# Kernel tuning notes

Measured on AMD Instinct MI355X. Metric: run time of the kernel, lower is better.

Reference implementation:

```python
import jax, jax.numpy as jnp
import numpy as np

B, T, I, H, L = 64, 1024, 64, 512, 2


def setup_inputs() -> dict:
    key = jax.random.key(0)
    ks = jax.random.split(key, 4 * L + 4)
    k = 1.0 / np.sqrt(H)
    inp = {"x": jax.random.normal(ks[0], (B, T, I), dtype=jnp.float32)}
    in_sizes = [I] + [H] * (L - 1)
    for l in range(L):
        base = 1 + 4 * l
        inp[f"w_ih{l}"] = jax.random.uniform(ks[base + 0], (3 * H, in_sizes[l]), minval=-k, maxval=k, dtype=jnp.float32)
        inp[f"w_hh{l}"] = jax.random.uniform(ks[base + 1], (3 * H, H), minval=-k, maxval=k, dtype=jnp.float32)
        inp[f"b_ih{l}"] = jax.random.uniform(ks[base + 2], (3 * H,), minval=-k, maxval=k, dtype=jnp.float32)
        inp[f"b_hh{l}"] = jax.random.uniform(ks[base + 3], (3 * H,), minval=-k, maxval=k, dtype=jnp.float32)
    kf = 1.0 / np.sqrt(H)
    inp["fc_w"] = jax.random.uniform(ks[-2], (I, H), minval=-kf, maxval=kf, dtype=jnp.float32)
    inp["fc_b"] = jax.random.uniform(ks[-1], (I,), minval=-kf, maxval=kf, dtype=jnp.float32)
    return inp


def _gru_layer(x, w_ih, w_hh, b_ih, b_hh):
    # x: [B, T, in]; precompute input-side gates as one big GEMM
    xg = jnp.einsum('bti,gi->btg', x, w_ih) + b_ih  # [B, T, 3H]
    h0 = jnp.zeros((x.shape[0], w_hh.shape[1]), x.dtype)

    def step(h, xg_t):
        hg = h @ w_hh.T + b_hh                     # [B, 3H]
        xr, xz, xn = jnp.split(xg_t, 3, axis=-1)
        hr, hz, hn = jnp.split(hg, 3, axis=-1)
        r = jax.nn.sigmoid(xr + hr)
        z = jax.nn.sigmoid(xz + hz)
        n = jnp.tanh(xn + r * hn)
        h_new = (1.0 - z) * n + z * h
        return h_new, h_new

    _, ys = jax.lax.scan(step, h0, jnp.swapaxes(xg, 0, 1))  # ys: [T, B, H]
    return jnp.swapaxes(ys, 0, 1)


def reference(x, w_ih0, w_hh0, b_ih0, b_hh0, w_ih1, w_hh1, b_ih1, b_hh1, fc_w, fc_b):
    h = _gru_layer(x, w_ih0, w_hh0, b_ih0, b_hh0)
    h = _gru_layer(h, w_ih1, w_hh1, b_ih1, b_hh1)
    return h @ fc_w.T + fc_b
```

## Files before the change

kernel.cpp:

```cpp
#include <hip/hip_runtime.h>
#include <hip/hip_bf16.h>

#define T_TOTAL 1024
#define BATCH   64
#define HID     512

__device__ __forceinline__ float fast_sigmoid(float x) {
    return 1.f / (1.f + __expf(-x));
}
__device__ __forceinline__ float fast_tanh(float x) {
    float ax = fabsf(x);
    float e  = __expf(-2.f * ax);
    float t  = (1.f - e) / (1.f + e);
    return copysignf(t, x);
}

template<int BM, int BN, int TM, int TN>
__global__ __launch_bounds__(256, 2)
void gemm_bt_k(const float* __restrict__ A, const float* __restrict__ W,
               const float* __restrict__ bias, float* __restrict__ C,
               int K, int T, int Tc, int t0, int N)
{
    constexpr int BK = 16;
    constexpr int WSTR = BN + (BN / 32) * 4;
    static_assert(BM / TM == 16 && BN / TN == 16, "256 threads required");
    __shared__ float As[BK][BM + 4];
    __shared__ float Ws[BK][WSTR];

    const int tid = threadIdx.x;
    const int tx  = tid & 15;
    const int ty  = tid >> 4;
    const int m0  = blockIdx.y * BM;
    const int n0  = blockIdx.x * BN;
    const int nA  = tx * TN;
    const int nsw = nA + ((nA >> 5) << 2);

    float acc[TM][TN];
#pragma unroll
    for (int i = 0; i < TM; ++i)
#pragma unroll
        for (int j = 0; j < TN; ++j) acc[i][j] = 0.f;

    for (int k0 = 0; k0 < K; k0 += BK) {
#pragma unroll
        for (int i = 0; i < (BM * BK) / 1024; ++i) {
            int id = tid + (i << 8);
            int m  = id >> 2;
            int kq = (id & 3) << 2;
            int mloc = m0 + m;
            int rowg = (mloc / Tc) * T + t0 + (mloc % Tc);
            const float4 v = *reinterpret_cast<const float4*>(A + (size_t)rowg * K + k0 + kq);
            As[kq + 0][m] = v.x; As[kq + 1][m] = v.y;
            As[kq + 2][m] = v.z; As[kq + 3][m] = v.w;
        }
#pragma unroll
        for (int i = 0; i < (BN * BK) / 1024; ++i) {
            int id = tid + (i << 8);
            int n  = id >> 2;
            int kq = (id & 3) << 2;
            const float4 v = *reinterpret_cast<const float4*>(W + (size_t)(n0 + n) * K + k0 + kq);
            int np = n + ((n >> 5) << 2);
            Ws[kq + 0][np] = v.x; Ws[kq + 1][np] = v.y;
            Ws[kq + 2][np] = v.z; Ws[kq + 3][np] = v.w;
        }
        __syncthreads();
#pragma unroll
        for (int k = 0; k < BK; ++k) {
            float a[TM], b[TN];
#pragma unroll
            for (int i = 0; i < TM; i += 4)
                *reinterpret_cast<float4*>(&a[i]) =
                    *reinterpret_cast<const float4*>(&As[k][ty * TM + i]);
#pragma unroll
            for (int j = 0; j < TN; j += 4)
                *reinterpret_cast<float4*>(&b[j]) =
                    *reinterpret_cast<const float4*>(&Ws[k][nsw + j]);
#pragma unroll
            for (int i = 0; i < TM; ++i)
#pragma unroll
                for (int j = 0; j < TN; ++j)
                    acc[i][j] = fmaf(a[i], b[j], acc[i][j]);
        }
        __syncthreads();
    }
#pragma unroll
    for (int i = 0; i < TM; ++i) {
        const size_t crow = (size_t)(m0 + ty * TM + i) * N + n0 + nA;
#pragma unroll
        for (int j = 0; j < TN; j += 4) {
            float4 bv = *reinterpret_cast<const float4*>(bias + n0 + nA + j);
            float4 v;
            v.x = acc[i][j + 0] + bv.x; v.y = acc[i][j + 1] + bv.y;
            v.z = acc[i][j + 2] + bv.z; v.w = acc[i][j + 3] + bv.w;
            *reinterpret_cast<float4*>(C + crow + j) = v;
        }
    }
}

__global__ __launch_bounds__(512, 2)
void gru_scan(const float* __restrict__ xg,
              const float* __restrict__ w_hh,
              const float* __restrict__ b_hh,
              float* __restrict__ y,
              unsigned long long* __restrict__ hbuf,
              int t0, int Tc, int tagbase)
{
    const int tid = threadIdx.x;
    const int grp = blockIdx.x & 31;
    const int os  = blockIdx.x >> 5;
    const int D0  = os << 6;
    const int d   = tid & 63;
    const int kc  = tid >> 6;
    const int bg  = grp << 1;

    __shared__ float h_lds[2][1024];
    __shared__ float part[2][8 * 392];

    float4 w4[3][16];
#pragma unroll
    for (int g = 0; g < 3; ++g) {
        const float* wr = w_hh + (size_t)(g * 512 + D0 + d) * 512 + kc * 64;
#pragma unroll
        for (int j = 0; j < 16; ++j)
            w4[g][j] = *reinterpret_cast<const float4*>(wr + (j << 2));
    }
    float bias_r = 0.f, bias_z = 0.f, bias_n = 0.f;
    if (tid < 128) {
        bias_r = b_hh[       D0 + d];
        bias_z = b_hh[ 512 + D0 + d];
        bias_n = b_hh[1024 + D0 + d];
    }
    const int b_loc = tid >> 6;

    for (int tl = 0; tl < Tc; ++tl) {
        const int tg = t0 + tl;
        float* hl = h_lds[tl & 1];
        float* pt = part[tl & 1];

        float xr = 0.f, xz = 0.f, xn = 0.f;
        if (tid < 128) {
            const size_t rowo = ((size_t)(bg + b_loc) * Tc + tl) * 1536 + D0 + d;
            xr = xg[rowo];
            xz = xg[rowo + 512];
            xn = xg[rowo + 1024];
        }

        if (tg == 0) {
            hl[      kc * 64 + d] = 0.f;
            hl[512 + kc * 64 + d] = 0.f;
        } else {
            const unsigned long long* hsrc =
                hbuf + (size_t)(grp * 2 + ((tg - 1) & 1)) * 1024 + kc * 64;
            const unsigned int tagexp = (unsigned int)(tagbase + tl - 1);
            unsigned long long v0, v1;
            for (;;) {
                v0 = __hip_atomic_load(hsrc + d,
                        __ATOMIC_RELAXED, __HIP_MEMORY_SCOPE_AGENT);
                v1 = __hip_atomic_load(hsrc + 512 + d,
                        __ATOMIC_RELAXED, __HIP_MEMORY_SCOPE_AGENT);
                const int ok = (int)(((unsigned int)(v0 >> 32) == tagexp) &
                                     ((unsigned int)(v1 >> 32) == tagexp));
                if (__all(ok)) break;
            }
            union { unsigned int u; float f; } c0, c1;
            c0.u = (unsigned int)v0;
            c1.u = (unsigned int)v1;
            hl[      kc * 64 + d] = c0.f;
            hl[512 + kc * 64 + d] = c1.f;
        }
        __builtin_amdgcn_s_waitcnt(0xC07F);

        float acc[3][2];
#pragma unroll
        for (int g = 0; g < 3; ++g) { acc[g][0] = 0.f; acc[g][1] = 0.f; }
        const float* hb = hl + kc * 64;
#pragma unroll
        for (int j = 0; j < 16; ++j) {
            const float4 h0 = *reinterpret_cast<const float4*>(hb + (j << 2));
            const float4 h1 = *reinterpret_cast<const float4*>(hb + 512 + (j << 2));
#pragma unroll
            for (int g = 0; g < 3; ++g) {
                const float4 wv = w4[g][j];
                acc[g][0] = fmaf(wv.x, h0.x, acc[g][0]);
                acc[g][0] = fmaf(wv.y, h0.y, acc[g][0]);
                acc[g][0] = fmaf(wv.z, h0.z, acc[g][0]);
                acc[g][0] = fmaf(wv.w, h0.w, acc[g][0]);
                acc[g][1] = fmaf(wv.x, h1.x, acc[g][1]);
                acc[g][1] = fmaf(wv.y, h1.y, acc[g][1]);
                acc[g][1] = fmaf(wv.z, h1.z, acc[g][1]);
                acc[g][1] = fmaf(wv.w, h1.w, acc[g][1]);
            }
        }
        {
            float* pp = pt + kc * 392 + d;
#pragma unroll
            for (int g = 0; g < 3; ++g) {
                pp[g * 128]      = acc[g][0];
                pp[g * 128 + 64] = acc[g][1];
            }
        }
        __syncthreads();

        if (tid < 128) {
            float sr = bias_r, sz = bias_z, sn = bias_n;
#pragma unroll
            for (int q = 0; q < 8; ++q) {
                sr += pt[q * 392 +       tid];
                sz += pt[q * 392 + 128 + tid];
                sn += pt[q * 392 + 256 + tid];
            }
            const int D = D0 + d;
            const float hp = hl[b_loc * 512 + D];
            const float r  = fast_sigmoid(xr + sr);
            const float z  = fast_sigmoid(xz + sz);
            const float nv = fast_tanh(xn + r * sn);
            const float h  = (1.f - z) * nv + z * hp;
            union { float f; unsigned int u; } cv; cv.f = h;
            const unsigned long long pk =
                ((unsigned long long)(unsigned int)(tagbase + tl) << 32) | cv.u;
            unsigned long long* hdst =
                hbuf + (size_t)(grp * 2 + (tg & 1)) * 1024 + b_loc * 512 + D;
            __hip_atomic_store(hdst, pk, __ATOMIC_RELAXED,
                               __HIP_MEMORY_SCOPE_AGENT);
            y[((size_t)(bg + b_loc) * T_TOTAL + tg) * HID + D] = h;
        }
    }
}

extern "C" void kernel_launch(void* const* d_in, const int* in_sizes, int n_in,
                              void* d_out, int out_size, void* d_ws, size_t ws_size,
                              hipStream_t stream)
{
    const float* x       = (const float*)d_in[0];
    const float* w_ih[2] = {(const float*)d_in[1], (const float*)d_in[5]};
    const float* w_hh[2] = {(const float*)d_in[2], (const float*)d_in[6]};
    const float* b_ih[2] = {(const float*)d_in[3], (const float*)d_in[7]};
    const float* b_hh[2] = {(const float*)d_in[4], (const float*)d_in[8]};
    const float* fc_w    = (const float*)d_in[9];
    const float* fc_b    = (const float*)d_in[10];
    float* out = (float*)d_out;

    const size_t Y_BYTES = (size_t)BATCH * T_TOTAL * HID * 4;
    const size_t H_BYTES = (size_t)32 * 2 * 2 * 512 * 8;
    int Tc = 256;
    while (Tc > 32) {
        size_t need = (size_t)BATCH * Tc * 1536 * 4 + Y_BYTES + H_BYTES;
        if (need <= ws_size) break;
        Tc >>= 1;
    }

    char* p = (char*)d_ws;
    float* xg_buf = (float*)p;                 p += (size_t)BATCH * Tc * 1536 * 4;
    float* y_buf  = (float*)p;                 p += Y_BYTES;
    unsigned long long* hbuf = (unsigned long long*)p;

    const int nchunks = T_TOTAL / Tc;
    for (int L = 0; L < 2; ++L) {
        const float* A = L ? y_buf : x;
        const int K    = L ? HID : 64;
        for (int c = 0; c < nchunks; ++c) {
            dim3 g1(1536 / 128, (BATCH * Tc) / 128);
            gemm_bt_k<128, 128, 8, 8><<<g1, 256, 0, stream>>>(
                A, w_ih[L], b_ih[L], xg_buf, K, T_TOTAL, Tc, c * Tc, 1536);
            gru_scan<<<256, 512, 0, stream>>>(
                xg_buf, w_hh[L], b_hh[L], y_buf, hbuf,
                c * Tc, Tc, (L << 11) + c * Tc);
        }
    }
    dim3 g2(64 / 64, (BATCH * T_TOTAL) / 128);
    gemm_bt_k<128, 64, 8, 4><<<g2, 256, 0, stream>>>(
        y_buf, fc_w, fc_b, out, HID, BATCH * T_TOTAL, BATCH * T_TOTAL, 0, 64);
}
```

Measured before the change: 6.125 ms.

## Double scan block size to split the K reduction across 16 warps

The recurrent scan now runs 1024 threads per block instead of 512. The hidden-state reduction dimension is split into 16 slices of 32 instead of 8 slices of 64, which halves the per-thread weight registers and the per-step FMA chain. Each thread polls one tagged hidden value instead of two. The cost is a larger shared partial-sum buffer, a 16-way reduction in the gate stage, and more waves competing per CU.

```diff
diff --git a/kernel.cpp b/kernel.cpp
--- a/kernel.cpp
+++ b/kernel.cpp
@@ -97,7 +97,7 @@
     }
 }
 
-__global__ __launch_bounds__(512, 2)
+__global__ __launch_bounds__(1024, 4)
 void gru_scan(const float* __restrict__ xg,
               const float* __restrict__ w_hh,
               const float* __restrict__ b_hh,
@@ -110,18 +110,18 @@
     const int os  = blockIdx.x >> 5;
     const int D0  = os << 6;
     const int d   = tid & 63;
-    const int kc  = tid >> 6;
+    const int w   = tid >> 6;
     const int bg  = grp << 1;
 
     __shared__ float h_lds[2][1024];
-    __shared__ float part[2][8 * 392];
-
-    float4 w4[3][16];
+    __shared__ float part[2][16 * 392];
+
+    float4 w4[3][8];
 #pragma unroll
     for (int g = 0; g < 3; ++g) {
-        const float* wr = w_hh + (size_t)(g * 512 + D0 + d) * 512 + kc * 64;
-#pragma unroll
-        for (int j = 0; j < 16; ++j)
+        const float* wr = w_hh + (size_t)(g * 512 + D0 + d) * 512 + 32 * w;
+#pragma unroll
+        for (int j = 0; j < 8; ++j)
             w4[g][j] = *reinterpret_cast<const float4*>(wr + (j << 2));
     }
     float bias_r = 0.f, bias_z = 0.f, bias_n = 0.f;
@@ -130,7 +130,9 @@
         bias_z = b_hh[ 512 + D0 + d];
         bias_n = b_hh[1024 + D0 + d];
     }
-    const int b_loc = tid >> 6;
+
+    const int pb   = d >> 5;
+    const int pdim = 32 * w + (d & 31);
 
     for (int tl = 0; tl < Tc; ++tl) {
         const int tg = t0 + tl;
@@ -139,43 +141,36 @@
 
         float xr = 0.f, xz = 0.f, xn = 0.f;
         if (tid < 128) {
-            const size_t rowo = ((size_t)(bg + b_loc) * Tc + tl) * 1536 + D0 + d;
+            const size_t rowo = ((size_t)(bg + w) * Tc + tl) * 1536 + D0 + d;
             xr = xg[rowo];
             xz = xg[rowo + 512];
             xn = xg[rowo + 1024];
         }
 
         if (tg == 0) {
-            hl[      kc * 64 + d] = 0.f;
-            hl[512 + kc * 64 + d] = 0.f;
+            hl[pb * 512 + pdim] = 0.f;
         } else {
             const unsigned long long* hsrc =
-                hbuf + (size_t)(grp * 2 + ((tg - 1) & 1)) * 1024 + kc * 64;
+                hbuf + (size_t)(grp * 2 + ((tg - 1) & 1)) * 1024 + pb * 512 + pdim;
             const unsigned int tagexp = (unsigned int)(tagbase + tl - 1);
-            unsigned long long v0, v1;
+            unsigned long long v0;
             for (;;) {
-                v0 = __hip_atomic_load(hsrc + d,
+                v0 = __hip_atomic_load(hsrc,
                         __ATOMIC_RELAXED, __HIP_MEMORY_SCOPE_AGENT);
-                v1 = __hip_atomic_load(hsrc + 512 + d,
-                        __ATOMIC_RELAXED, __HIP_MEMORY_SCOPE_AGENT);
-                const int ok = (int)(((unsigned int)(v0 >> 32) == tagexp) &
-                                     ((unsigned int)(v1 >> 32) == tagexp));
+                const int ok = (int)((unsigned int)(v0 >> 32) == tagexp);
                 if (__all(ok)) break;
             }
-            union { unsigned int u; float f; } c0, c1;
-            c0.u = (unsigned int)v0;
-            c1.u = (unsigned int)v1;
-            hl[      kc * 64 + d] = c0.f;
-            hl[512 + kc * 64 + d] = c1.f;
+            union { unsigned int u; float f; } c0; c0.u = (unsigned int)v0;
+            hl[pb * 512 + pdim] = c0.f;
         }
         __builtin_amdgcn_s_waitcnt(0xC07F);
 
         float acc[3][2];
 #pragma unroll
         for (int g = 0; g < 3; ++g) { acc[g][0] = 0.f; acc[g][1] = 0.f; }
-        const float* hb = hl + kc * 64;
-#pragma unroll
-        for (int j = 0; j < 16; ++j) {
+        const float* hb = hl + 32 * w;
+#pragma unroll
+        for (int j = 0; j < 8; ++j) {
             const float4 h0 = *reinterpret_cast<const float4*>(hb + (j << 2));
             const float4 h1 = *reinterpret_cast<const float4*>(hb + 512 + (j << 2));
 #pragma unroll
@@ -192,7 +187,7 @@
             }
         }
         {
-            float* pp = pt + kc * 392 + d;
+            float* pp = pt + w * 392 + d;
 #pragma unroll
             for (int g = 0; g < 3; ++g) {
                 pp[g * 128]      = acc[g][0];
@@ -204,13 +199,13 @@
         if (tid < 128) {
             float sr = bias_r, sz = bias_z, sn = bias_n;
 #pragma unroll
-            for (int q = 0; q < 8; ++q) {
+            for (int q = 0; q < 16; ++q) {
                 sr += pt[q * 392 +       tid];
                 sz += pt[q * 392 + 128 + tid];
                 sn += pt[q * 392 + 256 + tid];
             }
             const int D = D0 + d;
-            const float hp = hl[b_loc * 512 + D];
+            const float hp = hl[w * 512 + D];
             const float r  = fast_sigmoid(xr + sr);
             const float z  = fast_sigmoid(xz + sz);
             const float nv = fast_tanh(xn + r * sn);
@@ -219,10 +214,10 @@
             const unsigned long long pk =
                 ((unsigned long long)(unsigned int)(tagbase + tl) << 32) | cv.u;
             unsigned long long* hdst =
-                hbuf + (size_t)(grp * 2 + (tg & 1)) * 1024 + b_loc * 512 + D;
+                hbuf + (size_t)(grp * 2 + (tg & 1)) * 1024 + w * 512 + D;
             __hip_atomic_store(hdst, pk, __ATOMIC_RELAXED,
                                __HIP_MEMORY_SCOPE_AGENT);
-            y[((size_t)(bg + b_loc) * T_TOTAL + tg) * HID + D] = h;
+            y[((size_t)(bg + w) * T_TOTAL + tg) * HID + D] = h;
         }
     }
 }
@@ -262,7 +257,7 @@
             dim3 g1(1536 / 128, (BATCH * Tc) / 128);
             gemm_bt_k<128, 128, 8, 8><<<g1, 256, 0, stream>>>(
                 A, w_ih[L], b_ih[L], xg_buf, K, T_TOTAL, Tc, c * Tc, 1536);
-            gru_scan<<<256, 512, 0, stream>>>(
+            gru_scan<<<256, 1024, 0, stream>>>(
                 xg_buf, w_hh[L], b_hh[L], y_buf, hbuf,
                 c * Tc, Tc, (L << 11) + c * Tc);
         }
```

Measured after the change: 8.919 ms. +45.6%, slower.

## Wavefront-pipeline the two GRU layers so their chunk scans run concurrently

Applied to the files above, without the earlier changes.

Layer 1's recurrent scan on chunk s-1 now runs in the same launch as layer 0's scan on chunk s. A combined kernel dispatches 512 blocks, with each half handling one layer through a shared scan body. Separate xg and h-exchange buffers are allocated for each layer. This is meant to roughly halve the serial chain of time-step scans. The cost is double workspace and two blocks per CU contending for compute and LDS, and the spin-based cross-block sync relies on all 512 blocks being co-resident.

```diff
diff --git a/kernel.cpp b/kernel.cpp
--- a/kernel.cpp
+++ b/kernel.cpp
@@ -97,17 +97,18 @@
     }
 }
 
-__global__ __launch_bounds__(512, 2)
-void gru_scan(const float* __restrict__ xg,
-              const float* __restrict__ w_hh,
-              const float* __restrict__ b_hh,
-              float* __restrict__ y,
-              unsigned long long* __restrict__ hbuf,
-              int t0, int Tc, int tagbase)
+__device__ __forceinline__
+void scan_body(int bid,
+               const float* __restrict__ xg,
+               const float* __restrict__ w_hh,
+               const float* __restrict__ b_hh,
+               float* __restrict__ y,
+               unsigned long long* __restrict__ hbuf,
+               int t0, int Tc, int tagbase)
 {
     const int tid = threadIdx.x;
-    const int grp = blockIdx.x & 31;
-    const int os  = blockIdx.x >> 5;
+    const int grp = bid & 31;
+    const int os  = bid >> 5;
     const int D0  = os << 6;
     const int d   = tid & 63;
     const int kc  = tid >> 6;
@@ -227,6 +228,26 @@
     }
 }
 
+__global__ __launch_bounds__(512, 2)
+void gru_scan2(const float* __restrict__ xgA, const float* __restrict__ xgB,
+               const float* __restrict__ whhA, const float* __restrict__ whhB,
+               const float* __restrict__ bhhA, const float* __restrict__ bhhB,
+               float* __restrict__ y,
+               unsigned long long* __restrict__ hbufA,
+               unsigned long long* __restrict__ hbufB,
+               int t0A, int t0B, int tagA, int tagB, int Tc)
+{
+    const int half = blockIdx.x >> 8;
+    const int bid  = blockIdx.x & 255;
+    const float* xg  = half ? xgB  : xgA;
+    const float* whh = half ? whhB : whhA;
+    const float* bhh = half ? bhhB : bhhA;
+    unsigned long long* hb = half ? hbufB : hbufA;
+    const int t0 = half ? t0B  : t0A;
+    const int tb = half ? tagB : tagA;
+    scan_body(bid, xg, whh, bhh, y, hb, t0, Tc, tb);
+}
+
 extern "C" void kernel_launch(void* const* d_in, const int* in_sizes, int n_in,
                               void* d_out, int out_size, void* d_ws, size_t ws_size,
                               hipStream_t stream)
@@ -244,29 +265,49 @@
     const size_t H_BYTES = (size_t)32 * 2 * 2 * 512 * 8;
     int Tc = 256;
     while (Tc > 32) {
-        size_t need = (size_t)BATCH * Tc * 1536 * 4 + Y_BYTES + H_BYTES;
+        size_t need = 2 * (size_t)BATCH * Tc * 1536 * 4 + Y_BYTES + 2 * H_BYTES;
         if (need <= ws_size) break;
         Tc >>= 1;
     }
 
     char* p = (char*)d_ws;
-    float* xg_buf = (float*)p;                 p += (size_t)BATCH * Tc * 1536 * 4;
-    float* y_buf  = (float*)p;                 p += Y_BYTES;
-    unsigned long long* hbuf = (unsigned long long*)p;
+    float* xgA = (float*)p;                    p += (size_t)BATCH * Tc * 1536 * 4;
+    float* xgB = (float*)p;                    p += (size_t)BATCH * Tc * 1536 * 4;
+    float* y_buf = (float*)p;                  p += Y_BYTES;
+    unsigned long long* hbufA = (unsigned long long*)p;  p += H_BYTES;
+    unsigned long long* hbufB = (unsigned long long*)p;
 
     const int nchunks = T_TOTAL / Tc;
-    for (int L = 0; L < 2; ++L) {
-        const float* A = L ? y_buf : x;
-        const int K    = L ? HID : 64;
-        for (int c = 0; c < nchunks; ++c) {
-            dim3 g1(1536 / 128, (BATCH * Tc) / 128);
-            gemm_bt_k<128, 128, 8, 8><<<g1, 256, 0, stream>>>(
-                A, w_ih[L], b_ih[L], xg_buf, K, T_TOTAL, Tc, c * Tc, 1536);
-            gru_scan<<<256, 512, 0, stream>>>(
-                xg_buf, w_hh[L], b_hh[L], y_buf, hbuf,
-                c * Tc, Tc, (L << 11) + c * Tc);
-        }
-    }
+    dim3 gg(1536 / 128, (BATCH * Tc) / 128);
+
+    for (int s = 0; s <= nchunks; ++s) {
+        const bool hasA = (s < nchunks);
+        const bool hasB = (s >= 1);
+        if (hasA)
+            gemm_bt_k<128, 128, 8, 8><<<gg, 256, 0, stream>>>(
+                x, w_ih[0], b_ih[0], xgA, 64, T_TOTAL, Tc, s * Tc, 1536);
+        if (hasB)
+            gemm_bt_k<128, 128, 8, 8><<<gg, 256, 0, stream>>>(
+                y_buf, w_ih[1], b_ih[1], xgB, HID, T_TOTAL, Tc, (s - 1) * Tc, 1536);
+
+        if (hasA && hasB) {
+            gru_scan2<<<512, 512, 0, stream>>>(
+                xgA, xgB, w_hh[0], w_hh[1], b_hh[0], b_hh[1], y_buf,
+                hbufA, hbufB,
+                s * Tc, (s - 1) * Tc,
+                s * Tc, (1 << 11) + (s - 1) * Tc, Tc);
+        } else if (hasA) {
+            gru_scan2<<<256, 512, 0, stream>>>(
+                xgA, xgA, w_hh[0], w_hh[0], b_hh[0], b_hh[0], y_buf,
+                hbufA, hbufA, s * Tc, s * Tc, s * Tc, s * Tc, Tc);
+        } else {
+            gru_scan2<<<256, 512, 0, stream>>>(
+                xgB, xgB, w_hh[1], w_hh[1], b_hh[1], b_hh[1], y_buf,
+                hbufB, hbufB, (s - 1) * Tc, (s - 1) * Tc,
+                (1 << 11) + (s - 1) * Tc, (1 << 11) + (s - 1) * Tc, Tc);
+        }
+    }
+
     dim3 g2(64 / 64, (BATCH * T_TOTAL) / 128);
     gemm_bt_k<128, 64, 8, 4><<<g2, 256, 0, stream>>>(
         y_buf, fc_w, fc_b, out, HID, BATCH * T_TOTAL, BATCH * T_TOTAL, 0, 64);
```

Measured after the change: 6.520 ms. 6.4% more time.
